# Kernel tuning notes

Hardware: AMD Instinct MI355X
Metric: run time of the kernel (lower is better)

## Reference

```python
import jax, jax.numpy as jnp
import numpy as np

D, H, K = 384, 6, 8
B, NQ, NK = 4, 2048, 2048
EPS = 1e-5


def _ln(x, s, b):
    m = jnp.mean(x, axis=-1, keepdims=True)
    v = jnp.mean((x - m) ** 2, axis=-1, keepdims=True)
    return (x - m) * jax.lax.rsqrt(v + EPS) * s + b


def _mha(q, k, v, Wo, bo):
    # q,k,v: [B, N, D]
    dh = D // H
    qh = q.reshape(q.shape[0], q.shape[1], H, dh).transpose(0, 2, 1, 3)
    kh = k.reshape(k.shape[0], k.shape[1], H, dh).transpose(0, 2, 1, 3)
    vh = v.reshape(v.shape[0], v.shape[1], H, dh).transpose(0, 2, 1, 3)
    scores = jnp.einsum('bhqd,bhkd->bhqk', qh, kh) / jnp.sqrt(jnp.asarray(dh, q.dtype))
    attn = jax.nn.softmax(scores, axis=-1)
    out = jnp.einsum('bhqk,bhkd->bhqd', attn, vh)
    out = out.transpose(0, 2, 1, 3).reshape(q.shape[0], q.shape[1], D)
    return out @ Wo + bo


def _knn_edge(q_coords, k_coords, q_feats, k_feats):
    # coords: [B, N, 3]; feats: [B, N, D]. EdgeConv-style feature:
    # concat(neighbor_feat - center_feat, center_feat) -> [B, Nq, K, 2D]
    d2 = (jnp.sum(q_coords ** 2, -1)[:, :, None]
          + jnp.sum(k_coords ** 2, -1)[:, None, :]
          - 2.0 * jnp.einsum('bqc,bkc->bqk', q_coords, k_coords))
    _, idx = jax.lax.top_k(-d2, K)  # [B, Nq, K] nearest neighbors in key set
    neigh = jax.vmap(lambda f, i: f[i])(k_feats, idx)  # [B, Nq, K, D]
    center = jnp.broadcast_to(q_feats[:, :, None, :], neigh.shape)
    return jnp.concatenate([neigh - center, center], axis=-1)


def setup_inputs() -> dict:
    key = jax.random.key(0)
    ks = jax.random.split(key, 24)
    s = 0.02
    return {
        'query_points': jax.random.normal(ks[0], (B, 3 + D, NQ), jnp.float32),
        'key_points': jax.random.normal(ks[1], (B, 3 + D, NK), jnp.float32),
        'ln_in_s': jnp.ones((D,), jnp.float32), 'ln_in_b': jnp.zeros((D,), jnp.float32),
        'qkv_W': jax.random.normal(ks[2], (D, 3 * D), jnp.float32) * s,
        'attn_out_W': jax.random.normal(ks[3], (D, D), jnp.float32) * s,
        'attn_out_b': jnp.zeros((D,), jnp.float32),
        'ff_W1': jax.random.normal(ks[4], (D, 2 * D), jnp.float32) * s,
        'ff_b1': jnp.zeros((2 * D,), jnp.float32),
        'ff_W2': jax.random.normal(ks[5], (2 * D, D), jnp.float32) * s,
        'ff_b2': jnp.zeros((D,), jnp.float32),
        'ffn_s': jnp.ones((D,), jnp.float32), 'ffn_b': jnp.zeros((D,), jnp.float32),
        'knn1_W': jax.random.normal(ks[6], (2 * D, D), jnp.float32) * s,
        'knn1_b': jnp.zeros((D,), jnp.float32),
        'knn2_W': jax.random.normal(ks[7], (2 * D, D), jnp.float32) * s,
        'knn2_b': jnp.zeros((D,), jnp.float32),
        'self_merge_W': jax.random.normal(ks[8], (2 * D, D), jnp.float32) * s,
        'self_merge_b': jnp.zeros((D,), jnp.float32),
        'cross_merge_W': jax.random.normal(ks[9], (2 * D, D), jnp.float32) * s,
        'cross_merge_b': jnp.zeros((D,), jnp.float32),
        'cnq_s': jnp.ones((D,), jnp.float32), 'cnq_b': jnp.zeros((D,), jnp.float32),
        'cnk_s': jnp.ones((D,), jnp.float32), 'cnk_b': jnp.zeros((D,), jnp.float32),
        'cq_W': jax.random.normal(ks[10], (D, D), jnp.float32) * s,
        'ck_W': jax.random.normal(ks[11], (D, D), jnp.float32) * s,
        'cv_W': jax.random.normal(ks[12], (D, D), jnp.float32) * s,
    }


def reference(query_points, key_points, ln_in_s, ln_in_b, qkv_W, attn_out_W,
              attn_out_b, ff_W1, ff_b1, ff_W2, ff_b2, ffn_s, ffn_b,
              knn1_W, knn1_b, knn2_W, knn2_b, self_merge_W, self_merge_b,
              cross_merge_W, cross_merge_b, cnq_s, cnq_b, cnk_s, cnk_b,
              cq_W, ck_W, cv_W):
    qp = jnp.transpose(query_points, (0, 2, 1))  # [B, Nq, 3+D]
    kp = jnp.transpose(key_points, (0, 2, 1))    # [B, Nk, 3+D]
    q_coords, q_feats = qp[..., :3], qp[..., 3:]
    k_coords, k_feats = kp[..., :3], kp[..., 3:]

    # --- self attention + self kNN geometry ---
    norm_f = _ln(q_feats, ln_in_s, ln_in_b)
    qkv = norm_f @ qkv_W
    q, k, v = jnp.split(qkv, 3, axis=-1)
    attn_f = _mha(q, k, v, attn_out_W, attn_out_b)

    edge = _knn_edge(q_coords, q_coords, norm_f, norm_f)          # [B,Nq,K,2D]
    geom = jax.nn.leaky_relu(edge @ knn1_W + knn1_b, 0.2)
    geom = jnp.max(geom, axis=2)                                   # [B,Nq,D]

    attn_f = jnp.concatenate([attn_f, geom], axis=-1) @ self_merge_W + self_merge_b
    q_feats = attn_f + q_feats

    # --- cross attention + cross kNN geometry ---
    nq = _ln(q_feats, cnq_s, cnq_b)
    nk = _ln(k_feats, cnk_s, cnk_b)
    cross_f = _mha(nq @ cq_W, nk @ ck_W, nk @ cv_W, attn_out_W, attn_out_b)

    cedge = _knn_edge(q_coords, k_coords, nq, nk)                  # [B,Nq,K,2D]
    cgeom = jax.nn.leaky_relu(cedge @ knn2_W + knn2_b, 0.2)
    cgeom = jnp.max(cgeom, axis=2)

    cross_f = jnp.concatenate([cross_f, cgeom], axis=-1) @ cross_merge_W + cross_merge_b
    q_feats = q_feats + cross_f

    # --- feed forward ---
    h = _ln(q_feats, ffn_s, ffn_b)
    q_feats = q_feats + (jax.nn.gelu(h @ ff_W1 + ff_b1) @ ff_W2 + ff_b2)

    out = jnp.concatenate([q_coords, q_feats], axis=-1)
    return jnp.transpose(out, (0, 2, 1))  # [B, 3+D, Nq]
```

## Files before the change

kernel.cpp:

```cpp
#include <hip/hip_runtime.h>
#include <cstdint>
#include <cstddef>

#define NB 4
#define NN 2048
#define DD 384
#define NH 6

typedef float f4 __attribute__((ext_vector_type(4)));
typedef float f32x4 __attribute__((ext_vector_type(4)));
typedef short bf16x8 __attribute__((ext_vector_type(8)));
typedef unsigned u32x2 __attribute__((ext_vector_type(2)));

__device__ __forceinline__ float gelu_t(float x) {
  float x3 = x*x*x;
  return 0.5f*x*(1.0f + tanhf(0.7978845608028654f*(x + 0.044715f*x3)));
}

__device__ __forceinline__ unsigned short f2b(float f) {
  unsigned u = __builtin_bit_cast(unsigned, f);
  u += 0x7fffu + ((u >> 16) & 1u);
  return (unsigned short)(u >> 16);
}

__device__ __forceinline__ float b2f(unsigned short u) {
  return __builtin_bit_cast(float, ((unsigned)u) << 16);
}

__device__ __forceinline__ unsigned cvtpk(float a, float b) {
  unsigned r;
  asm("v_cvt_pk_bf16_f32 %0, %1, %2" : "=v"(r) : "v"(a), "v"(b));
  return r;
}

typedef __attribute__((address_space(1))) const void gvoid_t;
typedef __attribute__((address_space(3))) void lvoid_t;
__device__ __forceinline__ void gl16(const void* g, void* l) {
  __builtin_amdgcn_global_load_lds((gvoid_t*)g, (lvoid_t*)l, 16, 0, 0);
}

__device__ __forceinline__ unsigned long long shfl_xor_u64(unsigned long long v, int m) {
  unsigned lo = (unsigned)v, hi = (unsigned)(v >> 32);
  lo = (unsigned)__shfl_xor((int)lo, m);
  hi = (unsigned)__shfl_xor((int)hi, m);
  return ((unsigned long long)hi << 32) | lo;
}

__global__ __launch_bounds__(256) void split_k(const float* __restrict__ pts,
                                               float* __restrict__ coords,
                                               float* __restrict__ feats) {
  __shared__ float t[32][33];
  int b = blockIdx.z;
  int c0 = blockIdx.x*32, n0 = blockIdx.y*32;
  int tx = threadIdx.x, ty = threadIdx.y;
#pragma unroll
  for (int i = 0; i < 4; ++i) {
    int c = c0 + ty + i*8;
    if (c < 387) t[ty+i*8][tx] = pts[((size_t)b*387 + c)*NN + n0 + tx];
  }
  __syncthreads();
#pragma unroll
  for (int i = 0; i < 4; ++i) {
    int n = n0 + ty + i*8;
    int c = c0 + tx;
    if (c < 387) {
      float v = t[tx][ty+i*8];
      if (c < 3) coords[((size_t)b*NN + n)*4 + c] = v;
      else       feats[((size_t)b*NN + n)*DD + (c-3)] = v;
    }
    if (c0 == 0 && tx == 3) {
      float x = t[0][ty+i*8], y = t[1][ty+i*8], z = t[2][ty+i*8];
      coords[((size_t)b*NN + n)*4 + 3] = x*x + y*y + z*z;
    }
  }
}

__global__ __launch_bounds__(256) void pack_k(const float* __restrict__ coords,
                                              const float* __restrict__ feats,
                                              float* __restrict__ out) {
  __shared__ float t[32][33];
  int b = blockIdx.z;
  int c0 = blockIdx.x*32, n0 = blockIdx.y*32;
  int tx = threadIdx.x, ty = threadIdx.y;
#pragma unroll
  for (int i = 0; i < 4; ++i) {
    int n = n0 + ty + i*8;
    int c = c0 + tx;
    if (c < 387) {
      float v = (c < 3) ? coords[((size_t)b*NN + n)*4 + c]
                        : feats[((size_t)b*NN + n)*DD + (c-3)];
      t[tx][ty+i*8] = v;
    }
  }
  __syncthreads();
#pragma unroll
  for (int i = 0; i < 4; ++i) {
    int c = c0 + ty + i*8;
    if (c < 387) out[((size_t)b*387 + c)*NN + n0 + tx] = t[ty+i*8][tx];
  }
}

__device__ __forceinline__ void ln_body(const float* __restrict__ x,
                                        const float* __restrict__ g,
                                        const float* __restrict__ bb,
                                        unsigned short* __restrict__ o,
                                        int row) {
  int lane = threadIdx.x & 63;
  const float* xr = x + (size_t)row*DD;
  float v[6]; float s = 0.f;
#pragma unroll
  for (int i = 0; i < 6; ++i) { v[i] = xr[lane + i*64]; s += v[i]; }
#pragma unroll
  for (int off = 1; off < 64; off <<= 1) s += __shfl_xor(s, off);
  float mean = s * (1.f/384.f);
  float s2 = 0.f;
#pragma unroll
  for (int i = 0; i < 6; ++i) { float d = v[i] - mean; s2 += d*d; }
#pragma unroll
  for (int off = 1; off < 64; off <<= 1) s2 += __shfl_xor(s2, off);
  float rs = rsqrtf(s2*(1.f/384.f) + 1e-5f);
  unsigned short* orow = o + (size_t)row*DD;
#pragma unroll
  for (int i = 0; i < 6; ++i) {
    int c = lane + i*64;
    orow[c] = f2b((v[i]-mean)*rs*g[c] + bb[c]);
  }
}

__global__ __launch_bounds__(256) void ln_k(const float* __restrict__ x,
                                            const float* __restrict__ g,
                                            const float* __restrict__ bb,
                                            unsigned short* __restrict__ o) {
  ln_body(x, g, bb, o, blockIdx.x*4 + (threadIdx.x >> 6));
}

__global__ __launch_bounds__(256) void ln2_k(const float* __restrict__ x1,
                                             const float* __restrict__ g1,
                                             const float* __restrict__ b1,
                                             unsigned short* __restrict__ o1,
                                             const float* __restrict__ x2,
                                             const float* __restrict__ g2,
                                             const float* __restrict__ b2,
                                             unsigned short* __restrict__ o2) {
  int row = blockIdx.x*4 + (threadIdx.x >> 6);
  if (blockIdx.y == 0) ln_body(x1, g1, b1, o1, row);
  else                 ln_body(x2, g2, b2, o2, row);
}

struct WSrcs { const float* p[13]; };

__global__ __launch_bounds__(256) void wtrans_k(WSrcs srcs, unsigned short* __restrict__ dst) {
  constexpr int KK[13]  = {384,384,384,384,768,384,384,384,384,384,768,384,768};
  constexpr int NW[13]  = {1152,384,384,384,384,384,384,384,384,384,384,768,384};
  constexpr int MD[13]  = {0,0,2,0,0,0,0,0,0,2,0,0,0};
  constexpr int OFF[13] = {0,442368,589824,737280,884736,1179648,1327104,1474560,
                           1622016,1769472,1916928,2211840,2506752};
  constexpr int PFX[14] = {0,432,576,720,864,1152,1296,1440,1584,1728,1872,2160,2448,2736};
  int bid = blockIdx.x;
  int e = 0;
  while (bid >= PFX[e+1]) ++e;
  int t = bid - PFX[e];
  int K = KK[e], N = NW[e];
  int ntiles = N >> 5;
  int kt = t / ntiles, nt = t - kt*ntiles;
  const float* src = srcs.p[e];
  __shared__ float T[32][33];
  int tx = threadIdx.x & 31, ty = threadIdx.x >> 5;
  int n = nt*32 + tx;
#pragma unroll
  for (int i = 0; i < 4; ++i) {
    int k = kt*32 + ty + i*8;
    float v = src[(size_t)k*N + n];
    if (MD[e] == 2) v = src[(size_t)(k+384)*N + n] - v;
    T[ty+i*8][tx] = v;
  }
  __syncthreads();
#pragma unroll
  for (int i = 0; i < 4; ++i) {
    int nn = nt*32 + ty + i*8;
    int kk = kt*32 + tx;
    dst[(size_t)OFF[e] + (size_t)nn*K + kk] = f2b(T[tx][ty+i*8]);
  }
}

template<int ACT, int ACC, int OB, int HALFM>
__device__ __forceinline__ void mgemm_body(const unsigned short* __restrict__ A, int lda,
                                           const unsigned short* __restrict__ Wt,
                                           const float* __restrict__ bias,
                                           void* __restrict__ Cv, int ldc, int cofs,
                                           int Kd, int bx, int by, char* lds) {
  constexpr int BM   = HALFM ? 64 : 128;
  constexpr int MT   = HALFM ? 2 : 4;
  constexpr int AG   = HALFM ? 2 : 4;
  constexpr int ABUF = BM*128;
  constexpr int BUFSZ = ABUF + 8192;
  int tid = threadIdx.x;
  int lane = tid & 63, w = tid >> 6, g = lane >> 4, c = lane & 15;
  int wr = w >> 1, wc = w & 1;
  int m0 = by*BM, n0 = bx*64;
  int lrow = lane >> 3;
  int cswz = ((lane & 7) ^ lrow)*8;

  f32x4 acc[MT][2];
#pragma unroll
  for (int mt = 0; mt < MT; ++mt)
#pragma unroll
    for (int nt = 0; nt < 2; ++nt) acc[mt][nt] = 0.f;

  int KT = Kd >> 6;
  {
    char* As = lds; char* Bs = lds + ABUF;
#pragma unroll
    for (int i = 0; i < AG; ++i) {
      int rb = i*32 + w*8;
      gl16(A + (size_t)(m0 + rb + lrow)*lda + cswz, As + rb*128);
    }
#pragma unroll
    for (int i = 0; i < 2; ++i) {
      int rb = i*32 + w*8;
      gl16(Wt + (size_t)(n0 + rb + lrow)*Kd + cswz, Bs + rb*128);
    }
  }
  __syncthreads();

  for (int kt = 0; kt < KT; ++kt) {
    char* Asc = lds + (kt & 1)*BUFSZ;
    char* Bsc = Asc + ABUF;
    if (kt + 1 < KT) {
      char* Asn = lds + ((kt + 1) & 1)*BUFSZ;
      char* Bsn = Asn + ABUF;
      int k0 = (kt + 1)*64;
#pragma unroll
      for (int i = 0; i < AG; ++i) {
        int rb = i*32 + w*8;
        gl16(A + (size_t)(m0 + rb + lrow)*lda + k0 + cswz, Asn + rb*128);
      }
#pragma unroll
      for (int i = 0; i < 2; ++i) {
        int rb = i*32 + w*8;
        gl16(Wt + (size_t)(n0 + rb + lrow)*Kd + k0 + cswz, Bsn + rb*128);
      }
    }
#pragma unroll
    for (int kb = 0; kb < 2; ++kb) {
      bf16x8 af[MT], bfr[2];
#pragma unroll
      for (int mt = 0; mt < MT; ++mt) {
        int row = wr*(BM/2) + mt*16 + c;
        int ch = (kb*4 + g) ^ (row & 7);
        af[mt] = *(const bf16x8*)(Asc + row*128 + ch*16);
      }
#pragma unroll
      for (int nt = 0; nt < 2; ++nt) {
        int row = wc*32 + nt*16 + c;
        int ch = (kb*4 + g) ^ (row & 7);
        bfr[nt] = *(const bf16x8*)(Bsc + row*128 + ch*16);
      }
#pragma unroll
      for (int mt = 0; mt < MT; ++mt)
#pragma unroll
        for (int nt = 0; nt < 2; ++nt)
          acc[mt][nt] = __builtin_amdgcn_mfma_f32_16x16x32_bf16(af[mt], bfr[nt], acc[mt][nt], 0, 0, 0);
    }
    __syncthreads();
  }

#pragma unroll
  for (int mt = 0; mt < MT; ++mt) {
#pragma unroll
    for (int nt = 0; nt < 2; ++nt) {
      int coln = n0 + wc*32 + nt*16 + c;
      float bval = bias ? bias[coln] : 0.f;
#pragma unroll
      for (int r = 0; r < 4; ++r) {
        int m = m0 + wr*(BM/2) + mt*16 + 4*g + r;
        float t = acc[mt][nt][r] + bval;
        if (ACT == 1) t = gelu_t(t);
        if (OB) {
          ((unsigned short*)Cv)[(size_t)m*ldc + cofs + coln] = f2b(t);
        } else {
          float* cp = (float*)Cv + (size_t)m*ldc + cofs + coln;
          if (ACC) t += *cp;
          *cp = t;
        }
      }
    }
  }
}

template<int ACT, int ACC, int OB, int HALFM>
__global__ __launch_bounds__(256) void mgemm_k(const unsigned short* __restrict__ A, int lda,
                                               const unsigned short* __restrict__ Wt,
                                               const float* __restrict__ bias,
                                               void* __restrict__ Cv, int ldc, int cofs,
                                               int Kd) {
  constexpr int BM = HALFM ? 64 : 128;
  __shared__ char lds[2*(BM*128 + 8192)];
  mgemm_body<ACT,ACC,OB,HALFM>(A, lda, Wt, bias, Cv, ldc, cofs, Kd,
                               blockIdx.x, blockIdx.y, lds);
}

struct FSegs {
  const unsigned short* A[5];
  unsigned short* out[5];
  int ldc[5];
  int cofs[5];
};

__global__ __launch_bounds__(256) void fgemm_k(FSegs fs, const unsigned short* __restrict__ Wt) {
  __shared__ char lds[49152];
  int tid = threadIdx.x;
  int lane = tid & 63, w = tid >> 6, g = lane >> 4, c = lane & 15;
  int wr = w >> 1, wc = w & 1;
  int m0 = blockIdx.y*128, n0 = blockIdx.x*64;
  int seg = n0 / 384;
  const unsigned short* A = fs.A[seg];
  int lrow = lane >> 3;
  int cswz = ((lane & 7) ^ lrow)*8;

  f32x4 acc[4][2];
#pragma unroll
  for (int mt = 0; mt < 4; ++mt)
#pragma unroll
    for (int nt = 0; nt < 2; ++nt) acc[mt][nt] = 0.f;

  {
    char* As = lds; char* Bs = lds + 16384;
#pragma unroll
    for (int i = 0; i < 4; ++i) {
      int rb = i*32 + w*8;
      gl16(A + (size_t)(m0 + rb + lrow)*384 + cswz, As + rb*128);
    }
#pragma unroll
    for (int i = 0; i < 2; ++i) {
      int rb = i*32 + w*8;
      gl16(Wt + (size_t)(n0 + rb + lrow)*384 + cswz, Bs + rb*128);
    }
  }
  __syncthreads();

  for (int kt = 0; kt < 6; ++kt) {
    char* Asc = lds + (kt & 1)*24576;
    char* Bsc = Asc + 16384;
    if (kt + 1 < 6) {
      char* Asn = lds + ((kt + 1) & 1)*24576;
      char* Bsn = Asn + 16384;
      int k0 = (kt + 1)*64;
#pragma unroll
      for (int i = 0; i < 4; ++i) {
        int rb = i*32 + w*8;
        gl16(A + (size_t)(m0 + rb + lrow)*384 + k0 + cswz, Asn + rb*128);
      }
#pragma unroll
      for (int i = 0; i < 2; ++i) {
        int rb = i*32 + w*8;
        gl16(Wt + (size_t)(n0 + rb + lrow)*384 + k0 + cswz, Bsn + rb*128);
      }
    }
#pragma unroll
    for (int kb = 0; kb < 2; ++kb) {
      bf16x8 af[4], bfr[2];
#pragma unroll
      for (int mt = 0; mt < 4; ++mt) {
        int row = wr*64 + mt*16 + c;
        int ch = (kb*4 + g) ^ (row & 7);
        af[mt] = *(const bf16x8*)(Asc + row*128 + ch*16);
      }
#pragma unroll
      for (int nt = 0; nt < 2; ++nt) {
        int row = wc*32 + nt*16 + c;
        int ch = (kb*4 + g) ^ (row & 7);
        bfr[nt] = *(const bf16x8*)(Bsc + row*128 + ch*16);
      }
#pragma unroll
      for (int mt = 0; mt < 4; ++mt)
#pragma unroll
        for (int nt = 0; nt < 2; ++nt)
          acc[mt][nt] = __builtin_amdgcn_mfma_f32_16x16x32_bf16(af[mt], bfr[nt], acc[mt][nt], 0, 0, 0);
    }
    __syncthreads();
  }

  if (seg == 2) {
    unsigned short* vtp = fs.out[2];
    int bb = m0 >> 11;
    int tokb = (m0 & 2047) + wr*64 + 4*g;
#pragma unroll
    for (int mt = 0; mt < 4; ++mt) {
#pragma unroll
      for (int nt = 0; nt < 2; ++nt) {
        int cseg = (n0 - 768) + wc*32 + nt*16 + c;
        int h = cseg >> 6, d = cseg & 63;
        u32x2 pv;
        pv[0] = cvtpk(acc[mt][nt][0], acc[mt][nt][1]);
        pv[1] = cvtpk(acc[mt][nt][2], acc[mt][nt][3]);
        *(u32x2*)(vtp + ((size_t)((bb*NH + h)*64 + d))*NN + tokb + mt*16) = pv;
      }
    }
    return;
  }

  float qs = (seg == 0) ? 0.18033688011112042f : 1.0f;
  unsigned short* outp = fs.out[seg];
  int ldcs = fs.ldc[seg];
  int cbase = fs.cofs[seg] + (n0 - seg*384);
#pragma unroll
  for (int mt = 0; mt < 4; ++mt) {
#pragma unroll
    for (int nt = 0; nt < 2; ++nt) {
      int coln = cbase + wc*32 + nt*16 + c;
#pragma unroll
      for (int r = 0; r < 4; ++r) {
        int m = m0 + wr*64 + mt*16 + 4*g + r;
        outp[(size_t)m*ldcs + coln] = f2b(acc[mt][nt][r]*qs);
      }
    }
  }
}

__global__ __launch_bounds__(256) void flashm_k(const unsigned short* __restrict__ qkvb,
                                                const unsigned short* __restrict__ vt,
                                                unsigned short* __restrict__ o) {
  __shared__ char smem[49152];
  char* PT = smem + 32768;
  int bid = blockIdx.x;
  int s = (bid & 7)*48 + (bid >> 3);
  int qt = s & 15; int hb = s >> 4;
  int h = hb % NH, b = hb / NH;
  int q0 = qt*128;
  int tid = threadIdx.x;
  int w = tid >> 6, lane = tid & 63, g = lane >> 4, c = lane & 15;
  int lrow = lane >> 3;
  int gsw = ((lane & 7) ^ lrow)*8;

  const unsigned short* kbase = qkvb + (size_t)b*NN*1152 + 384 + h*64;
  const unsigned short* vbase = vt + ((size_t)(b*NH + h))*64*NN;

  bf16x8 qfA[2], qfB[2];
  {
    const unsigned short* qa = qkvb + ((size_t)(b*NN + q0 + w*32 + c))*1152 + h*64;
    const unsigned short* qb = qa + (size_t)16*1152;
    qfA[0] = *(const bf16x8*)(qa + 8*g);
    qfA[1] = *(const bf16x8*)(qa + 32 + 8*g);
    qfB[0] = *(const bf16x8*)(qb + 8*g);
    qfB[1] = *(const bf16x8*)(qb + 32 + 8*g);
  }
  bf16x8 onesv;
#pragma unroll
  for (int i = 0; i < 8; ++i) onesv[i] = (short)0x3F80;

  f32x4 oaccA[4], oaccB[4];
#pragma unroll
  for (int i = 0; i < 4; ++i) { oaccA[i] = 0.f; oaccB[i] = 0.f; }
  f32x4 laccA = 0.f, laccB = 0.f;

#define FSTAGE(bf, ktb) { \
    char* KB = smem + (bf)*16384; char* VB = KB + 8192; \
    gl16(kbase + (size_t)((ktb)*64 + w*16 + lrow)*1152 + gsw,     KB + (w*16)*128); \
    gl16(kbase + (size_t)((ktb)*64 + w*16 + 8 + lrow)*1152 + gsw, KB + (w*16+8)*128); \
    gl16(vbase + (size_t)(w*16 + lrow)*NN + (ktb)*64 + gsw,       VB + (w*16)*128); \
    gl16(vbase + (size_t)(w*16 + 8 + lrow)*NN + (ktb)*64 + gsw,   VB + (w*16+8)*128); }

  FSTAGE(0, 0);
  __syncthreads();

  for (int kt = 0; kt < 32; ++kt) {
    if (kt + 1 < 32) FSTAGE((kt + 1) & 1, kt + 1);
    char* KTc = smem + (kt & 1)*16384;
    char* VTc = KTc + 8192;

    f32x4 sTa[4], sTb[4];
#pragma unroll
    for (int nt = 0; nt < 4; ++nt) { sTa[nt] = 0.f; sTb[nt] = 0.f; }
#pragma unroll
    for (int nt = 0; nt < 4; ++nt) {
      int krow = nt*16 + c;
#pragma unroll
      for (int kb = 0; kb < 2; ++kb) {
        int ch = ((kb*4 + g) ^ (krow & 7))*16;
        bf16x8 kf_ = *(const bf16x8*)(KTc + krow*128 + ch);
        sTa[nt] = __builtin_amdgcn_mfma_f32_16x16x32_bf16(kf_, qfA[kb], sTa[nt], 0, 0, 0);
        sTb[nt] = __builtin_amdgcn_mfma_f32_16x16x32_bf16(kf_, qfB[kb], sTb[nt], 0, 0, 0);
      }
    }

    int prowA = w*32 + c;
    int prowB = prowA + 16;
    int pswz = (c & 7) << 4;
#pragma unroll
    for (int nt = 0; nt < 4; ++nt) {
      float a0 = __builtin_amdgcn_exp2f(sTa[nt][0]);
      float a1 = __builtin_amdgcn_exp2f(sTa[nt][1]);
      float a2 = __builtin_amdgcn_exp2f(sTa[nt][2]);
      float a3 = __builtin_amdgcn_exp2f(sTa[nt][3]);
      u32x2 pka;
      pka[0] = cvtpk(a0, a1);
      pka[1] = cvtpk(a2, a3);
      *(u32x2*)(PT + prowA*128 + ((nt*32 + 8*g) ^ pswz)) = pka;
      float b0 = __builtin_amdgcn_exp2f(sTb[nt][0]);
      float b1 = __builtin_amdgcn_exp2f(sTb[nt][1]);
      float b2 = __builtin_amdgcn_exp2f(sTb[nt][2]);
      float b3 = __builtin_amdgcn_exp2f(sTb[nt][3]);
      u32x2 pkb;
      pkb[0] = cvtpk(b0, b1);
      pkb[1] = cvtpk(b2, b3);
      *(u32x2*)(PT + prowB*128 + ((nt*32 + 8*g) ^ pswz)) = pkb;
    }

    bf16x8 pbA[2], pbB[2];
#pragma unroll
    for (int kb = 0; kb < 2; ++kb) {
      int ch = ((kb*4 + g) ^ (c & 7))*16;
      pbA[kb] = *(const bf16x8*)(PT + prowA*128 + ch);
      pbB[kb] = *(const bf16x8*)(PT + prowB*128 + ch);
    }

    laccA = __builtin_amdgcn_mfma_f32_16x16x32_bf16(onesv, pbA[0], laccA, 0, 0, 0);
    laccA = __builtin_amdgcn_mfma_f32_16x16x32_bf16(onesv, pbA[1], laccA, 0, 0, 0);
    laccB = __builtin_amdgcn_mfma_f32_16x16x32_bf16(onesv, pbB[0], laccB, 0, 0, 0);
    laccB = __builtin_amdgcn_mfma_f32_16x16x32_bf16(onesv, pbB[1], laccB, 0, 0, 0);

#pragma unroll
    for (int dt = 0; dt < 4; ++dt) {
      int vrow = dt*16 + c;
#pragma unroll
      for (int kb = 0; kb < 2; ++kb) {
        int ch = ((kb*4 + g) ^ (vrow & 7))*16;
        bf16x8 vf = *(const bf16x8*)(VTc + vrow*128 + ch);
        oaccA[dt] = __builtin_amdgcn_mfma_f32_16x16x32_bf16(vf, pbA[kb], oaccA[dt], 0, 0, 0);
        oaccB[dt] = __builtin_amdgcn_mfma_f32_16x16x32_bf16(vf, pbB[kb], oaccB[dt], 0, 0, 0);
      }
    }
    __syncthreads();
  }
#undef FSTAGE

  float invA = 1.f / laccA[0];
  float invB = 1.f / laccB[0];
  size_t orowA = ((size_t)b*NN + q0 + w*32 + c)*DD + h*64;
  size_t orowB = orowA + (size_t)16*DD;
#pragma unroll
  for (int dt = 0; dt < 4; ++dt) {
    u32x2 ova, ovb;
    ova[0] = cvtpk(oaccA[dt][0]*invA, oaccA[dt][1]*invA);
    ova[1] = cvtpk(oaccA[dt][2]*invA, oaccA[dt][3]*invA);
    *(u32x2*)(o + orowA + dt*16 + 4*g) = ova;
    ovb[0] = cvtpk(oaccB[dt][0]*invB, oaccB[dt][1]*invB);
    ovb[1] = cvtpk(oaccB[dt][2]*invB, oaccB[dt][3]*invB);
    *(u32x2*)(o + orowB + dt*16 + 4*g) = ovb;
  }
}

__global__ __launch_bounds__(256) void knn2_k(const float* __restrict__ qc4,
                                              const float* __restrict__ kc4,
                                              int* __restrict__ idx1,
                                              int* __restrict__ idx2) {
  __shared__ unsigned long long sbuf[4][64];
  const float* kcs = blockIdx.y ? kc4 : qc4;
  int* idxo = blockIdx.y ? idx2 : idx1;
  int lane = threadIdx.x & 63;
  int w = threadIdx.x >> 6;
  int q = blockIdx.x*4 + w;
  int b = q >> 11;
  f4 qv = *(const f4*)(qc4 + (size_t)q*4);
  float mx_ = -2.f*qv[0], my_ = -2.f*qv[1], mz_ = -2.f*qv[2];
  const float* kb = kcs + (size_t)b*NN*4;

  float fv[32];
  float fm = INFINITY;
#pragma unroll
  for (int i = 0; i < 32; ++i) {
    f4 kv = *(const f4*)(kb + (size_t)(lane + i*64)*4);
    float f = fmaf(mx_, kv[0], fmaf(my_, kv[1], fmaf(mz_, kv[2], kv[3])));
    fv[i] = f;
    fm = fminf(fm, f);
  }

  {
    float v = fm;
#pragma unroll
    for (int k = 2; k <= 64; k <<= 1) {
#pragma unroll
      for (int j = k >> 1; j >= 1; j >>= 1) {
        float p = __shfl_xor(v, j);
        bool tmin = (((lane & k) == 0) == ((lane & j) == 0));
        v = tmin ? fminf(v, p) : fmaxf(v, p);
      }
    }
    fm = __shfl(v, 7);
  }
  float T = fm;

  int cnt = 0;
#pragma unroll
  for (int i = 0; i < 32; ++i) {
    bool p = fv[i] <= T;
    unsigned long long mask = __ballot(p);
    if (mask) {
      if (p) {
        int off = cnt + (int)__popcll(mask & ((1ull << lane) - 1ull));
        unsigned u = __builtin_bit_cast(unsigned, fv[i]);
        u ^= 0x80000000u | (unsigned)((int)u >> 31);
        if (off < 64)
          sbuf[w][off] = ((unsigned long long)u << 32) | (unsigned)(lane + i*64);
      }
      cnt += (int)__popcll(mask);
    }
  }

  unsigned long long key = ~0ull;
  if (lane < cnt && lane < 64) key = sbuf[w][lane];
#pragma unroll
  for (int k = 2; k <= 64; k <<= 1) {
#pragma unroll
    for (int j = k >> 1; j >= 1; j >>= 1) {
      unsigned long long p = shfl_xor_u64(key, j);
      bool tmin = (((lane & k) == 0) == ((lane & j) == 0));
      bool less = key < p;
      unsigned long long mn = less ? key : p;
      unsigned long long mx = less ? p : key;
      key = tmin ? mn : mx;
    }
  }
  if (lane < 8) idxo[(size_t)q*8 + lane] = (int)(unsigned)key;
}

__device__ __forceinline__ void geom_body(const unsigned short* __restrict__ GCb,
                                          const float* __restrict__ bias,
                                          const int* __restrict__ idx,
                                          unsigned short* __restrict__ out,
                                          int q) {
  int b = q >> 11;
  int t = threadIdx.x;
  int j[8];
#pragma unroll
  for (int k = 0; k < 8; ++k) j[k] = idx[(size_t)q*8 + k];
  const unsigned short* base = GCb + ((size_t)(b << 11))*768;
  {
    float c = b2f(GCb[(size_t)q*768 + 384 + t]) + bias[t];
    float mx = -INFINITY;
#pragma unroll
    for (int k = 0; k < 8; ++k) {
      float y = b2f(base[(size_t)j[k]*768 + t]) + c;
      y = (y > 0.f) ? y : 0.2f*y;
      mx = fmaxf(mx, y);
    }
    out[(size_t)q*768 + 384 + t] = f2b(mx);
  }
  if (t < 128) {
    int d = t + 256;
    float c = b2f(GCb[(size_t)q*768 + 384 + d]) + bias[d];
    float mx = -INFINITY;
#pragma unroll
    for (int k = 0; k < 8; ++k) {
      float y = b2f(base[(size_t)j[k]*768 + d]) + c;
      y = (y > 0.f) ? y : 0.2f*y;
      mx = fmaxf(mx, y);
    }
    out[(size_t)q*768 + 384 + d] = f2b(mx);
  }
}

__global__ __launch_bounds__(256) void wog_k(const unsigned short* __restrict__ A,
                                             const unsigned short* __restrict__ Wt,
                                             const float* __restrict__ wob,
                                             unsigned short* __restrict__ attnG,
                                             const unsigned short* __restrict__ GCb,
                                             const float* __restrict__ gbias,
                                             const int* __restrict__ idx) {
  __shared__ char lds[32768];
  int bid = blockIdx.x;
  int gq;
  if (bid < 8448) {
    int t = bid / 11, r = bid - t*11;
    if (r == 0) {
      mgemm_body<0,0,1,1>(A, 384, Wt, wob, attnG, 768, 0, 384, t % 6, t / 6, lds);
      return;
    }
    gq = t*10 + (r - 1);
  } else {
    gq = 7680 + (bid - 8448);
  }
  geom_body(GCb, gbias, idx, attnG, gq);
}

extern "C" void kernel_launch(void* const* d_in, const int* in_sizes, int n_in,
                              void* d_out, int out_size, void* d_ws, size_t ws_size,
                              hipStream_t stream) {
  (void)in_sizes; (void)n_in; (void)out_size; (void)ws_size;
  const float* qpts  = (const float*)d_in[0];
  const float* kpts  = (const float*)d_in[1];
  const float* ln_s  = (const float*)d_in[2];
  const float* ln_b  = (const float*)d_in[3];
  const float* qkvW  = (const float*)d_in[4];
  const float* Wo    = (const float*)d_in[5];
  const float* bo    = (const float*)d_in[6];
  const float* ffW1  = (const float*)d_in[7];
  const float* ffb1  = (const float*)d_in[8];
  const float* ffW2  = (const float*)d_in[9];
  const float* ffb2  = (const float*)d_in[10];
  const float* ffns  = (const float*)d_in[11];
  const float* ffnb  = (const float*)d_in[12];
  const float* knn1W = (const float*)d_in[13];
  const float* knn1b = (const float*)d_in[14];
  const float* knn2W = (const float*)d_in[15];
  const float* knn2b = (const float*)d_in[16];
  const float* smW   = (const float*)d_in[17];
  const float* smb   = (const float*)d_in[18];
  const float* cmW   = (const float*)d_in[19];
  const float* cmb   = (const float*)d_in[20];
  const float* cnqs  = (const float*)d_in[21];
  const float* cnqb  = (const float*)d_in[22];
  const float* cnks  = (const float*)d_in[23];
  const float* cnkb  = (const float*)d_in[24];
  const float* cqW   = (const float*)d_in[25];
  const float* ckW   = (const float*)d_in[26];
  const float* cvW   = (const float*)d_in[27];

  float* ws = (float*)d_ws;
  float* qc4  = ws;
  float* kc4  = qc4 + 32768;
  float* qf   = kc4 + 32768;
  float* kf   = qf + 3145728;
  unsigned short* nrmb = (unsigned short*)(kf + 3145728);
  unsigned short* nkb  = (unsigned short*)(kf + 3145728 + 1572864);
  float* qkv = kf + 3145728 + 1572864 + 1572864;
  unsigned short* qkvb   = (unsigned short*)qkv;
  unsigned short* attnGb = (unsigned short*)qkv;
  unsigned short* vtb    = (unsigned short*)(qkv + 4718592);
  unsigned short* wtb    = (unsigned short*)(qkv + 4718592 + 1572864);
  unsigned short* attnOb = (unsigned short*)(qkv + 4718592 + 1572864 + 1400832);
  unsigned short* GCbb   = (unsigned short*)((float*)attnOb + 1572864);
  int* idx1 = (int*)((float*)GCbb + 3145728);
  int* idx2 = idx1 + 65536;

  const int W_FA=0, W_WO=737280, W_SM=884736, W_FB=1179648,
            W_CM=1916928, W_FF1=2211840, W_FF2=2506752;

  WSrcs srcs;
  srcs.p[0]=qkvW; srcs.p[1]=knn1W; srcs.p[2]=knn1W; srcs.p[3]=Wo; srcs.p[4]=smW;
  srcs.p[5]=cqW; srcs.p[6]=ckW; srcs.p[7]=cvW; srcs.p[8]=knn2W; srcs.p[9]=knn2W;
  srcs.p[10]=cmW; srcs.p[11]=ffW1; srcs.p[12]=ffW2;
  wtrans_k<<<2736, 256, 0, stream>>>(srcs, wtb);

  dim3 tgrid(13, 64, NB), tblk(32, 8);
  split_k<<<tgrid, tblk, 0, stream>>>(qpts, qc4, qf);
  split_k<<<tgrid, tblk, 0, stream>>>(kpts, kc4, kf);

  knn2_k<<<dim3(2048, 2), 256, 0, stream>>>(qc4, kc4, idx1, idx2);

  dim3 mg384h(6, 128), mg768(12, 64), fg(30, 64);

  ln_k<<<2048, 256, 0, stream>>>(qf, ln_s, ln_b, nrmb);
  {
    FSegs fa;
    for (int s = 0; s < 5; ++s) fa.A[s] = nrmb;
    fa.out[0] = qkvb; fa.ldc[0] = 1152; fa.cofs[0] = 0;
    fa.out[1] = qkvb; fa.ldc[1] = 1152; fa.cofs[1] = 384;
    fa.out[2] = vtb;  fa.ldc[2] = 0;    fa.cofs[2] = 0;
    fa.out[3] = GCbb; fa.ldc[3] = 768;  fa.cofs[3] = 0;
    fa.out[4] = GCbb; fa.ldc[4] = 768;  fa.cofs[4] = 384;
    fgemm_k<<<fg, 256, 0, stream>>>(fa, wtb + W_FA);
  }
  flashm_k<<<384, 256, 0, stream>>>(qkvb, vtb, attnOb);
  wog_k<<<8960, 256, 0, stream>>>(attnOb, wtb+W_WO, bo, attnGb, GCbb, knn1b, idx1);
  mgemm_k<0,1,0,1><<<mg384h, 256, 0, stream>>>(attnGb, 768, wtb+W_SM, smb, qf, DD, 0, 768);

  ln2_k<<<dim3(2048, 2), 256, 0, stream>>>(qf, cnqs, cnqb, nrmb, kf, cnks, cnkb, nkb);
  {
    FSegs fb;
    fb.A[0] = nrmb; fb.A[1] = nkb; fb.A[2] = nkb; fb.A[3] = nkb; fb.A[4] = nrmb;
    fb.out[0] = qkvb; fb.ldc[0] = 1152; fb.cofs[0] = 0;
    fb.out[1] = qkvb; fb.ldc[1] = 1152; fb.cofs[1] = 384;
    fb.out[2] = vtb;  fb.ldc[2] = 0;    fb.cofs[2] = 0;
    fb.out[3] = GCbb; fb.ldc[3] = 768;  fb.cofs[3] = 0;
    fb.out[4] = GCbb; fb.ldc[4] = 768;  fb.cofs[4] = 384;
    fgemm_k<<<fg, 256, 0, stream>>>(fb, wtb + W_FB);
  }
  flashm_k<<<384, 256, 0, stream>>>(qkvb, vtb, attnOb);
  wog_k<<<8960, 256, 0, stream>>>(attnOb, wtb+W_WO, bo, attnGb, GCbb, knn2b, idx2);
  mgemm_k<0,1,0,1><<<mg384h, 256, 0, stream>>>(attnGb, 768, wtb+W_CM, cmb, qf, DD, 0, 768);

  ln_k<<<2048, 256, 0, stream>>>(qf, ffns, ffnb, nrmb);
  mgemm_k<1,0,1,0><<<mg768, 256, 0, stream>>>(nrmb, DD, wtb+W_FF1, ffb1, attnGb, 768, 0, DD);
  mgemm_k<0,1,0,1><<<mg384h, 256, 0, stream>>>(attnGb, 768, wtb+W_FF2, ffb2, qf, DD, 0, 768);

  pack_k<<<tgrid, tblk, 0, stream>>>(qc4, qf, (float*)d_out);
}
```

Baseline: 321.9 us.

## Split flash attention over key range and combine partials in separate kernel

Each flash-attention block now handles half of the key tiles, so the grid doubles from 384 to 768 blocks to better fill the GPU's compute units. Unnormalized fp32 output accumulators and row sums are written to a workspace. A new combine kernel adds the two halves, normalizes and converts to bf16. Combining by plain sums relies on the existing softmax not using a per-block running max. The change adds a large fp32 partial-result write and read, plus an extra launch per attention call.

```diff
diff --git a/kernel.cpp b/kernel.cpp
--- a/kernel.cpp
+++ b/kernel.cpp
@@ -420,12 +420,13 @@
 
 __global__ __launch_bounds__(256) void flashm_k(const unsigned short* __restrict__ qkvb,
                                                 const unsigned short* __restrict__ vt,
-                                                unsigned short* __restrict__ o) {
+                                                float* __restrict__ pO,
+                                                float* __restrict__ pL) {
   __shared__ char smem[49152];
   char* PT = smem + 32768;
   int bid = blockIdx.x;
-  int s = (bid & 7)*48 + (bid >> 3);
-  int qt = s & 15; int hb = s >> 4;
+  int s = (bid & 7)*96 + (bid >> 3);
+  int qt = s & 15, sp = (s >> 4) & 1, hb = s >> 5;
   int h = hb % NH, b = hb / NH;
   int q0 = qt*128;
   int tid = threadIdx.x;
@@ -461,12 +462,13 @@
     gl16(vbase + (size_t)(w*16 + lrow)*NN + (ktb)*64 + gsw,       VB + (w*16)*128); \
     gl16(vbase + (size_t)(w*16 + 8 + lrow)*NN + (ktb)*64 + gsw,   VB + (w*16+8)*128); }
 
-  FSTAGE(0, 0);
+  int kt0 = sp*16;
+  FSTAGE(0, kt0);
   __syncthreads();
 
-  for (int kt = 0; kt < 32; ++kt) {
-    if (kt + 1 < 32) FSTAGE((kt + 1) & 1, kt + 1);
-    char* KTc = smem + (kt & 1)*16384;
+  for (int t2 = 0; t2 < 16; ++t2) {
+    if (t2 + 1 < 16) FSTAGE((t2 + 1) & 1, kt0 + t2 + 1);
+    char* KTc = smem + (t2 & 1)*16384;
     char* VTc = KTc + 8192;
 
     f32x4 sTa[4], sTb[4];
@@ -535,19 +537,42 @@
   }
 #undef FSTAGE
 
-  float invA = 1.f / laccA[0];
-  float invB = 1.f / laccB[0];
-  size_t orowA = ((size_t)b*NN + q0 + w*32 + c)*DD + h*64;
-  size_t orowB = orowA + (size_t)16*DD;
+  int blk = (hb*16 + qt)*2 + sp;
+  float* po = pO + (size_t)blk*8192;
+  int qA = w*32 + c, qB = qA + 16;
 #pragma unroll
   for (int dt = 0; dt < 4; ++dt) {
-    u32x2 ova, ovb;
-    ova[0] = cvtpk(oaccA[dt][0]*invA, oaccA[dt][1]*invA);
-    ova[1] = cvtpk(oaccA[dt][2]*invA, oaccA[dt][3]*invA);
-    *(u32x2*)(o + orowA + dt*16 + 4*g) = ova;
-    ovb[0] = cvtpk(oaccB[dt][0]*invB, oaccB[dt][1]*invB);
-    ovb[1] = cvtpk(oaccB[dt][2]*invB, oaccB[dt][3]*invB);
-    *(u32x2*)(o + orowB + dt*16 + 4*g) = ovb;
+    *(f4*)(po + qA*64 + dt*16 + 4*g) = oaccA[dt];
+    *(f4*)(po + qB*64 + dt*16 + 4*g) = oaccB[dt];
+  }
+  if (g == 0) {
+    pL[(size_t)blk*128 + qA] = laccA[0];
+    pL[(size_t)blk*128 + qB] = laccB[0];
+  }
+}
+
+__global__ __launch_bounds__(256) void comb_k(const float* __restrict__ pO,
+                                              const float* __restrict__ pL,
+                                              unsigned short* __restrict__ o) {
+  int blk = blockIdx.x;
+  int hb = blk >> 4, qt = blk & 15;
+  int h = hb % NH, b = hb / NH;
+  const float* p0 = pO + (size_t)blk*2*8192;
+  const float* p1 = p0 + 8192;
+  const float* l0 = pL + (size_t)blk*2*128;
+  int t = threadIdx.x;
+  int q = t >> 1, d0 = (t & 1)*32;
+  float inv = 1.f / (l0[q] + l0[128 + q]);
+  size_t orow = ((size_t)b*NN + qt*128 + q)*DD + h*64 + d0;
+#pragma unroll
+  for (int i = 0; i < 32; i += 4) {
+    f4 a = *(const f4*)(p0 + q*64 + d0 + i);
+    f4 bb = *(const f4*)(p1 + q*64 + d0 + i);
+    a = (a + bb)*inv;
+    u32x2 ov;
+    ov[0] = cvtpk(a[0], a[1]);
+    ov[1] = cvtpk(a[2], a[3]);
+    *(u32x2*)(o + orow + i) = ov;
   }
 }
 
@@ -733,6 +758,8 @@
   unsigned short* GCbb   = (unsigned short*)((float*)attnOb + 1572864);
   int* idx1 = (int*)((float*)GCbb + 3145728);
   int* idx2 = idx1 + 65536;
+  float* pO = (float*)(idx2 + 65536);
+  float* pL = pO + 6291456;
 
   const int W_FA=0, W_WO=737280, W_SM=884736, W_FB=1179648,
             W_CM=1916928, W_FF1=2211840, W_FF2=2506752;
@@ -762,7 +789,8 @@
     fa.out[4] = GCbb; fa.ldc[4] = 768;  fa.cofs[4] = 384;
     fgemm_k<<<fg, 256, 0, stream>>>(fa, wtb + W_FA);
   }
-  flashm_k<<<384, 256, 0, stream>>>(qkvb, vtb, attnOb);
+  flashm_k<<<768, 256, 0, stream>>>(qkvb, vtb, pO, pL);
+  comb_k<<<384, 256, 0, stream>>>(pO, pL, attnOb);
   wog_k<<<8960, 256, 0, stream>>>(attnOb, wtb+W_WO, bo, attnGb, GCbb, knn1b, idx1);
   mgemm_k<0,1,0,1><<<mg384h, 256, 0, stream>>>(attnGb, 768, wtb+W_SM, smb, qf, DD, 0, 768);
 
@@ -777,7 +805,8 @@
     fb.out[4] = GCbb; fb.ldc[4] = 768;  fb.cofs[4] = 384;
     fgemm_k<<<fg, 256, 0, stream>>>(fb, wtb + W_FB);
   }
-  flashm_k<<<384, 256, 0, stream>>>(qkvb, vtb, attnOb);
+  flashm_k<<<768, 256, 0, stream>>>(qkvb, vtb, pO, pL);
+  comb_k<<<384, 256, 0, stream>>>(pO, pL, attnOb);
   wog_k<<<8960, 256, 0, stream>>>(attnOb, wtb+W_WO, bo, attnGb, GCbb, knn2b, idx2);
   mgemm_k<0,1,0,1><<<mg384h, 256, 0, stream>>>(attnGb, 768, wtb+W_CM, cmb, qf, DD, 0, 768);
 
```

Result: slower. 331.7 us (+3.0%).
